# Performance work log

Measured on AMD Instinct MI355X. Metric: run time of the kernel, lower is better.

## Reference

```python
import jax, jax.numpy as jnp
import numpy as np

B, H, W, C = 8, 256, 256, 64
M1, M2 = 32, 32
SCALE = 1.0 / (C * C)


def setup_inputs() -> dict:
    key = jax.random.key(0)
    ku, k1, k2, k3, k4 = jax.random.split(key, 5)
    u = jax.random.normal(ku, (B, H, W, C), dtype=jnp.float32)
    wshape = (C, C, M1, M2)
    w_pos_r = SCALE * jax.random.normal(k1, wshape, dtype=jnp.float32)
    w_pos_i = SCALE * jax.random.normal(k2, wshape, dtype=jnp.float32)
    w_neg_r = SCALE * jax.random.normal(k3, wshape, dtype=jnp.float32)
    w_neg_i = SCALE * jax.random.normal(k4, wshape, dtype=jnp.float32)
    return {"u": u, "w_pos_r": w_pos_r, "w_pos_i": w_pos_i,
            "w_neg_r": w_neg_r, "w_neg_i": w_neg_i}


def _compl_mul2d(inp, weights):
    # inp: [B, m1, m2, Cin] complex; weights: [Cin, Cout, m1, m2] complex
    return jnp.einsum('bxyi,ioxy->bxyo', inp, weights)


def reference(u, w_pos_r, w_pos_i, w_neg_r, w_neg_i):
    b, h, w, c = u.shape
    wf = w // 2 + 1  # rfft size along W
    u_ft = jnp.fft.rfft2(u, axes=(1, 2))  # [B, H, Wf, C] complex
    w_pos = jax.lax.complex(w_pos_r, w_pos_i)
    w_neg = jax.lax.complex(w_neg_r, w_neg_i)
    top = _compl_mul2d(u_ft[:, :M1, :M2, :], w_pos)   # low positive freqs
    bot = _compl_mul2d(u_ft[:, h - M1:, :M2, :], w_neg)  # low negative freqs
    # out_ft zero-initialized, only truncated modes populated.
    # (Original allocates [B,H,W,C] but irfft2 with s=(H,W) only reads
    #  the first W//2+1 columns, which equals this [B,H,Wf,C] tensor.)
    out_ft = jnp.zeros((b, h, wf, c), dtype=u_ft.dtype)
    out_ft = out_ft.at[:, :M1, :M2, :].set(top)
    out_ft = out_ft.at[:, h - M1:, :M2, :].set(bot)
    # out_ft[:, -M1:M1] assignment in original is an empty slice (M1 <= H/2): no-op.
    return jnp.fft.irfft2(out_ft, s=(h, w), axes=(1, 2)).astype(u.dtype)
```

## Files before the change

### kernel.cpp

```cpp
#include <hip/hip_runtime.h>
#include <math.h>

#define BB 8
#define HH 256
#define WW 256
#define CC 64

__device__ inline void cmac(float2& a, float tx, float ty, float2 v) {
    a.x += tx * v.x - ty * v.y;
    a.y += tx * v.y + ty * v.x;
}
__device__ inline void fma4(float4& a, float s, float4 v) {
    a.x += s * v.x; a.y += s * v.y; a.z += s * v.z; a.w += s * v.w;
}

__global__ __launch_bounds__(256) void k_tw(float2* __restrict__ Tf,
                                            float2* __restrict__ Ti,
                                            float* __restrict__ Ty,
                                            float* __restrict__ T2) {
    int e = blockIdx.x * 256 + threadIdx.x;
    if (e < 16384) {
        int x = e >> 6;
        int j = e & 63;
        int kxa = j + ((j >> 5) * 192);
        int tt = (kxa * x) & 255;
        float ang = (float)tt * (6.283185307179586f / 256.0f);
        float s, c;
        sincosf(ang, &s, &c);
        Tf[(size_t)x * 64 + j] = make_float2(c, -s);
        const float k = 2.0f / 65536.0f;
        Ti[(size_t)j * 256 + x] = make_float2(c * k, s * k);
    } else {
        int f = e - 16384;
        if (f < 8192) {
            int yp = f >> 6;
            int col = f & 63;
            int par = (col >> 5) & 1;
            int cs = (col >> 4) & 1;
            int m = col & 15;
            int ky = 2 * m + par;
            int tt = (ky * yp) & 255;
            float ang = (float)tt * (6.283185307179586f / 256.0f);
            float s, c;
            sincosf(ang, &s, &c);
            Ty[f] = cs ? -s : c;
        } else {
            int g = f - 8192;
            int pi = g >> 12;
            int j = (g >> 7) & 31;
            int p = g & 127;
            int m = j >> 1, ri = j & 1;
            int ky = 2 * m + pi;
            int tt = (ky * p) & 255;
            float ang = (float)tt * (6.283185307179586f / 256.0f);
            float s, c;
            sincosf(ang, &s, &c);
            T2[g] = ri ? -s : c;
        }
    }
}

__global__ __launch_bounds__(256) void k_fwd_y(const float* __restrict__ u,
                                               const float* __restrict__ Ty,
                                               float2* __restrict__ V) {
    __shared__ float ue[4][16 * 68];
    __shared__ float uo[4][16 * 68];
    __shared__ float Tt[16 * 68];

    int t = threadIdx.x;
    int bx = blockIdx.x;
    int b = bx >> 6;
    int x4 = (bx & 63) * 4;
    int r = t >> 6;
    int l = t & 63;
    int x = x4 + r;
    int i8 = (l & 7) * 8;
    int w = l >> 3;
    int p = w & 1;
    int kq = w >> 1;
    int yy = l >> 2;
    int c0 = (l & 3) * 16;
    int trow = t >> 4;
    int tc = (t & 15) * 4;

    const float* ub = u + ((size_t)(b * HH + x)) * (WW * CC);
    const float* uplane = p ? uo[r] : ue[r];

    float4 aR[4], aI[4], bR[4], bI[4];
    #pragma unroll
    for (int m = 0; m < 4; ++m) {
        aR[m] = make_float4(0,0,0,0); aI[m] = make_float4(0,0,0,0);
        bR[m] = make_float4(0,0,0,0); bI[m] = make_float4(0,0,0,0);
    }

    for (int yt = 0; yt < 8; ++yt) {
        const float* plo = ub + (size_t)(yt * 16 + yy) * CC + c0;
        const float* phi = plo + 128 * CC;
        float4 l0 = *(const float4*)(plo);
        float4 l1 = *(const float4*)(plo + 4);
        float4 l2 = *(const float4*)(plo + 8);
        float4 l3 = *(const float4*)(plo + 12);
        float4 h0 = *(const float4*)(phi);
        float4 h1 = *(const float4*)(phi + 4);
        float4 h2 = *(const float4*)(phi + 8);
        float4 h3 = *(const float4*)(phi + 12);
        float4 tv = *(const float4*)(Ty + (size_t)(yt * 16 + trow) * 64 + tc);

        __syncthreads();
        int wb = yy * 68 + c0;
        float* uer = ue[r];
        float* uor = uo[r];
        *(float4*)(uer + wb)      = make_float4(l0.x+h0.x, l0.y+h0.y, l0.z+h0.z, l0.w+h0.w);
        *(float4*)(uer + wb + 4)  = make_float4(l1.x+h1.x, l1.y+h1.y, l1.z+h1.z, l1.w+h1.w);
        *(float4*)(uer + wb + 8)  = make_float4(l2.x+h2.x, l2.y+h2.y, l2.z+h2.z, l2.w+h2.w);
        *(float4*)(uer + wb + 12) = make_float4(l3.x+h3.x, l3.y+h3.y, l3.z+h3.z, l3.w+h3.w);
        *(float4*)(uor + wb)      = make_float4(l0.x-h0.x, l0.y-h0.y, l0.z-h0.z, l0.w-h0.w);
        *(float4*)(uor + wb + 4)  = make_float4(l1.x-h1.x, l1.y-h1.y, l1.z-h1.z, l1.w-h1.w);
        *(float4*)(uor + wb + 8)  = make_float4(l2.x-h2.x, l2.y-h2.y, l2.z-h2.z, l2.w-h2.w);
        *(float4*)(uor + wb + 12) = make_float4(l3.x-h3.x, l3.y-h3.y, l3.z-h3.z, l3.w-h3.w);
        *(float4*)(Tt + trow * 68 + tc) = tv;
        __syncthreads();

        #pragma unroll
        for (int y2 = 0; y2 < 16; ++y2) {
            const float* tb = Tt + y2 * 68 + p * 32 + kq * 2;
            float2 c01 = *(const float2*)(tb);
            float2 c89 = *(const float2*)(tb + 8);
            float2 s01 = *(const float2*)(tb + 16);
            float2 s89 = *(const float2*)(tb + 24);
            const float* up = uplane + y2 * 68 + i8;
            float4 u0 = *(const float4*)(up);
            float4 u1 = *(const float4*)(up + 4);
            fma4(aR[0], c01.x, u0);  fma4(bR[0], c01.x, u1);
            fma4(aI[0], s01.x, u0);  fma4(bI[0], s01.x, u1);
            fma4(aR[1], c01.y, u0);  fma4(bR[1], c01.y, u1);
            fma4(aI[1], s01.y, u0);  fma4(bI[1], s01.y, u1);
            fma4(aR[2], c89.x, u0);  fma4(bR[2], c89.x, u1);
            fma4(aI[2], s89.x, u0);  fma4(bI[2], s89.x, u1);
            fma4(aR[3], c89.y, u0);  fma4(bR[3], c89.y, u1);
            fma4(aI[3], s89.y, u0);  fma4(bI[3], s89.y, u1);
        }
    }

    int mv[4] = {2 * kq, 2 * kq + 1, 2 * kq + 8, 2 * kq + 9};
    #pragma unroll
    for (int mi = 0; mi < 4; ++mi) {
        int ky = 2 * mv[mi] + p;
        float2* vp = V + (size_t)(b * HH + x) * 2048 + ky * 64 + i8;
        *(float4*)(vp)     = make_float4(aR[mi].x, aI[mi].x, aR[mi].y, aI[mi].y);
        *(float4*)(vp + 2) = make_float4(aR[mi].z, aI[mi].z, aR[mi].w, aI[mi].w);
        *(float4*)(vp + 4) = make_float4(bR[mi].x, bI[mi].x, bR[mi].y, bI[mi].y);
        *(float4*)(vp + 6) = make_float4(bR[mi].z, bI[mi].z, bR[mi].w, bI[mi].w);
    }
}

__global__ __launch_bounds__(256) void k_fwd_x(const float2* __restrict__ Tf,
                                               const float2* __restrict__ V,
                                               float2* __restrict__ U) {
    __shared__ float sRe[2 * 2048];
    __shared__ float sIm[2 * 2048];
    __shared__ float2 Ts[32 * 16];

    int bx = blockIdx.x;
    int jq = bx >> 8;
    int ky = bx & 31;
    int b  = (bx >> 5) & 7;
    int t = threadIdx.x;
    int jr = t >> 5;
    int ir = t & 31;

    float2 a00 = {0,0}, a01 = {0,0}, a10 = {0,0}, a11 = {0,0};

    const float2* vb = V + (size_t)b * (HH * 2048) + ky * 64;
    int vrow = t >> 3;
    int vcol = (t & 7) * 8;
    int tjj = (t & 7) * 2;
    int parOff = (jr & 1) * 2048;

    for (int x0 = 0; x0 < 128; x0 += 32) {
        const float2* plo = vb + (size_t)(x0 + vrow) * 2048 + vcol;
        const float2* phi = plo + 128 * 2048;
        float4 l0 = *(const float4*)(plo);
        float4 l1 = *(const float4*)(plo + 2);
        float4 l2 = *(const float4*)(plo + 4);
        float4 l3 = *(const float4*)(plo + 6);
        float4 h0 = *(const float4*)(phi);
        float4 h1 = *(const float4*)(phi + 2);
        float4 h2 = *(const float4*)(phi + 4);
        float4 h3 = *(const float4*)(phi + 6);
        float4 tv = *(const float4*)(Tf + (size_t)(x0 + vrow) * 64 + jq * 16 + tjj);

        __syncthreads();
        *(float4*)&Ts[vrow * 16 + tjj] = tv;
        int wb = vrow * 64 + vcol;
        *(float4*)(sRe + wb)            = make_float4(l0.x+h0.x, l0.z+h0.z, l1.x+h1.x, l1.z+h1.z);
        *(float4*)(sRe + wb + 4)        = make_float4(l2.x+h2.x, l2.z+h2.z, l3.x+h3.x, l3.z+h3.z);
        *(float4*)(sIm + wb)            = make_float4(l0.y+h0.y, l0.w+h0.w, l1.y+h1.y, l1.w+h1.w);
        *(float4*)(sIm + wb + 4)        = make_float4(l2.y+h2.y, l2.w+h2.w, l3.y+h3.y, l3.w+h3.w);
        *(float4*)(sRe + 2048 + wb)     = make_float4(l0.x-h0.x, l0.z-h0.z, l1.x-h1.x, l1.z-h1.z);
        *(float4*)(sRe + 2048 + wb + 4) = make_float4(l2.x-h2.x, l2.z-h2.z, l3.x-h3.x, l3.z-h3.z);
        *(float4*)(sIm + 2048 + wb)     = make_float4(l0.y-h0.y, l0.w-h0.w, l1.y-h1.y, l1.w-h1.w);
        *(float4*)(sIm + 2048 + wb + 4) = make_float4(l2.y-h2.y, l2.w-h2.w, l3.y-h3.y, l3.w-h3.w);
        __syncthreads();

        #pragma unroll
        for (int xx = 0; xx < 32; ++xx) {
            float2 t0 = Ts[xx * 16 + jr];
            float2 t1 = Ts[xx * 16 + jr + 8];
            const float* re = sRe + parOff + xx * 64;
            const float* im = sIm + parOff + xx * 64;
            float vr0 = re[ir], vr1 = re[ir + 32];
            float vi0 = im[ir], vi1 = im[ir + 32];
            a00.x += t0.x*vr0 - t0.y*vi0;  a00.y += t0.x*vi0 + t0.y*vr0;
            a01.x += t0.x*vr1 - t0.y*vi1;  a01.y += t0.x*vi1 + t0.y*vr1;
            a10.x += t1.x*vr0 - t1.y*vi0;  a10.y += t1.x*vi0 + t1.y*vr0;
            a11.x += t1.x*vr1 - t1.y*vi1;  a11.y += t1.x*vi1 + t1.y*vr1;
        }
    }

    int j0 = jq * 16 + jr;
    float2* u0 = U + ((size_t)(j0 * 32 + ky) * 8 + b) * 64 + ir;
    u0[0]  = a00;
    u0[32] = a01;
    float2* u1 = U + ((size_t)((j0 + 8) * 32 + ky) * 8 + b) * 64 + ir;
    u1[0]  = a10;
    u1[32] = a11;
}

__global__ __launch_bounds__(256) void k_modew(const float* __restrict__ wpr,
                                               const float* __restrict__ wpi,
                                               const float* __restrict__ wnr,
                                               const float* __restrict__ wni,
                                               const float2* __restrict__ U,
                                               float2* __restrict__ OF) {
    __shared__ float2 uS[4 * 8 * 64];
    __shared__ float2 wS[4 * 8 * 32];

    int bx = blockIdx.x;
    int j   = bx & 63;
    int kyt = (bx >> 6) & 7;
    int oh  = bx >> 9;
    int ky0 = kyt * 4;
    int sel = j >> 5, kxl = j & 31;
    const float* sr = sel ? wnr : wpr;
    const float* si = sel ? wni : wpi;
    int tid = threadIdx.x;

    {
        const float4* up4 = (const float4*)(U + (size_t)(j * 32 + ky0) * 512);
        float4* uS4 = (float4*)uS;
        #pragma unroll
        for (int k = 0; k < 4; ++k) uS4[tid + 256 * k] = up4[tid + 256 * k];
    }

    int o32 = tid & 31;
    int bh  = tid >> 5;
    int irS = tid >> 5;
    int ooS = tid & 31;

    float2 acc[4];
    #pragma unroll
    for (int k = 0; k < 4; ++k) acc[k] = make_float2(0.f, 0.f);

    for (int it = 0; it < 8; ++it) {
        __syncthreads();
        {
            int ig = it * 8 + irS;
            int og = oh * 32 + ooS;
            size_t base = (((size_t)(ig * 64 + og)) * 32 + kxl) * 32 + ky0;
            float4 r0 = *(const float4*)(sr + base);
            float4 q0 = *(const float4*)(si + base);
            float2* wrow = wS + irS * 32 + ooS;
            wrow[0 * 256] = make_float2(r0.x, q0.x);
            wrow[1 * 256] = make_float2(r0.y, q0.y);
            wrow[2 * 256] = make_float2(r0.z, q0.z);
            wrow[3 * 256] = make_float2(r0.w, q0.w);
        }
        __syncthreads();
        #pragma unroll
        for (int ir = 0; ir < 8; ++ir) {
            int ig = it * 8 + ir;
            #pragma unroll
            for (int ky = 0; ky < 4; ++ky) {
                float2 wv = wS[ky * 256 + ir * 32 + o32];
                float2 uv = uS[ky * 512 + bh * 64 + ig];
                acc[ky].x += uv.x * wv.x - uv.y * wv.y;
                acc[ky].y += uv.x * wv.y + uv.y * wv.x;
            }
        }
    }

    int og = oh * 32 + o32;
    #pragma unroll
    for (int ky = 0; ky < 4; ++ky) {
        OF[((size_t)(bh * 32 + ky0 + ky) * 64 + j) * 64 + og] = acc[ky];
    }
}

__global__ __launch_bounds__(256) void k_inv_x(const float2* __restrict__ Ti,
                                               const float2* __restrict__ OF,
                                               float2* __restrict__ A) {
    __shared__ float2 Ts[32 * 32];
    __shared__ float2 Os[32 * 64];

    int bx = blockIdx.x;
    int xt = bx >> 8;
    int ky = bx & 31;
    int b  = (bx >> 5) & 7;
    int t = threadIdx.x;
    int or_ = t & 15;
    int xr = t >> 4;

    float2 acc[2][2][4];
    #pragma unroll
    for (int pa = 0; pa < 2; ++pa)
        #pragma unroll
        for (int p = 0; p < 2; ++p)
            #pragma unroll
            for (int q = 0; q < 4; ++q) acc[pa][p][q] = make_float2(0.f, 0.f);

    const float2* ofb = OF + (size_t)(b * 32 + ky) * 4096;
    int sj = t >> 3;
    int sx = (t & 7) * 4;
    int so = (t & 7) * 8;

    for (int kh = 0; kh < 2; ++kh) {
        const float2* tsrc = Ti + (size_t)(kh * 32 + sj) * 256 + xt * 32 + sx;
        float4 t0 = *(const float4*)(tsrc);
        float4 t1 = *(const float4*)(tsrc + 2);
        const float2* osrc = ofb + (size_t)(kh * 32 + sj) * 64 + so;
        float4 o0 = *(const float4*)(osrc);
        float4 o1 = *(const float4*)(osrc + 2);
        float4 o2 = *(const float4*)(osrc + 4);
        float4 o3 = *(const float4*)(osrc + 6);

        __syncthreads();
        *(float4*)&Ts[sj * 32 + sx]     = t0;
        *(float4*)&Ts[sj * 32 + sx + 2] = t1;
        float2* od = &Os[sj * 64 + so];
        *(float4*)(od)     = o0;
        *(float4*)(od + 2) = o1;
        *(float4*)(od + 4) = o2;
        *(float4*)(od + 6) = o3;
        __syncthreads();

        #pragma unroll
        for (int jj = 0; jj < 32; ++jj) {
            float4 tp = *(const float4*)&Ts[jj * 32 + xr * 2];
            float2 q0 = Os[jj * 64 + or_];
            float2 q1 = Os[jj * 64 + or_ + 16];
            float2 q2 = Os[jj * 64 + or_ + 32];
            float2 q3 = Os[jj * 64 + or_ + 48];
            const int pa = jj & 1;
            cmac(acc[pa][0][0], tp.x, tp.y, q0);
            cmac(acc[pa][0][1], tp.x, tp.y, q1);
            cmac(acc[pa][0][2], tp.x, tp.y, q2);
            cmac(acc[pa][0][3], tp.x, tp.y, q3);
            cmac(acc[pa][1][0], tp.z, tp.w, q0);
            cmac(acc[pa][1][1], tp.z, tp.w, q1);
            cmac(acc[pa][1][2], tp.z, tp.w, q2);
            cmac(acc[pa][1][3], tp.z, tp.w, q3);
        }
    }

    float sc = (ky == 0) ? 0.5f : 1.0f;
    #pragma unroll
    for (int p = 0; p < 2; ++p) {
        int x = xt * 32 + xr * 2 + p;
        float2* alo = A + ((size_t)(b * 256 + x) * 32 + ky) * 64 + or_;
        float2* ahi = A + ((size_t)(b * 256 + x + 128) * 32 + ky) * 64 + or_;
        #pragma unroll
        for (int q = 0; q < 4; ++q) {
            float2 se = acc[0][p][q], so2 = acc[1][p][q];
            alo[16 * q] = make_float2((se.x + so2.x) * sc, (se.y + so2.y) * sc);
            ahi[16 * q] = make_float2((se.x - so2.x) * sc, (se.y - so2.y) * sc);
        }
    }
}

__global__ __launch_bounds__(256) void k_inv_y(const float* __restrict__ T2g,
                                               const float2* __restrict__ A,
                                               float* __restrict__ out) {
    __shared__ float As[64 * 68];
    __shared__ float T2s[64 * 132];

    int t = threadIdx.x;
    int b = blockIdx.x >> 8;
    int x = blockIdx.x & 255;

    {
        int ky = t >> 3;
        int oc = (t & 7) * 8;
        const float2* ap = A + (size_t)(b * 256 + x) * 2048 + ky * 64 + oc;
        float4 g0 = *(const float4*)(ap);
        float4 g1 = *(const float4*)(ap + 2);
        float4 g2 = *(const float4*)(ap + 4);
        float4 g3 = *(const float4*)(ap + 6);
        int pi = ky & 1, m = ky >> 1;
        float* re = As + ((pi * 32) + 2 * m) * 68 + oc;
        float* im = As + ((pi * 32) + 2 * m + 1) * 68 + oc;
        *(float4*)(re)     = make_float4(g0.x, g0.z, g1.x, g1.z);
        *(float4*)(re + 4) = make_float4(g2.x, g2.z, g3.x, g3.z);
        *(float4*)(im)     = make_float4(g0.y, g0.w, g1.y, g1.w);
        *(float4*)(im + 4) = make_float4(g2.y, g2.w, g3.y, g3.w);
    }
    {
        int row = t >> 2;
        int c = (t & 3) * 32;
        const float* tg = T2g + (size_t)row * 128 + c;
        float* td = T2s + row * 132 + c;
        #pragma unroll
        for (int k = 0; k < 8; ++k) {
            float4 q = *(const float4*)(tg + 4 * k);
            *(float4*)(td + 4 * k) = q;
        }
    }
    __syncthreads();

    int pr = t >> 4;
    int o4 = (t & 15) * 4;

    float4 acc[2][8];
    #pragma unroll
    for (int pi = 0; pi < 2; ++pi)
        #pragma unroll
        for (int pp = 0; pp < 8; ++pp) acc[pi][pp] = make_float4(0,0,0,0);

    #pragma unroll
    for (int pi = 0; pi < 2; ++pi) {
        #pragma unroll
        for (int jj = 0; jj < 32; ++jj) {
            const float* trow = T2s + (pi * 32 + jj) * 132 + pr * 8;
            float4 ta = *(const float4*)(trow);
            float4 tb = *(const float4*)(trow + 4);
            float4 av = *(const float4*)(As + (pi * 32 + jj) * 68 + o4);
            fma4(acc[pi][0], ta.x, av);
            fma4(acc[pi][1], ta.y, av);
            fma4(acc[pi][2], ta.z, av);
            fma4(acc[pi][3], ta.w, av);
            fma4(acc[pi][4], tb.x, av);
            fma4(acc[pi][5], tb.y, av);
            fma4(acc[pi][6], tb.z, av);
            fma4(acc[pi][7], tb.w, av);
        }
    }

    float* op = out + (size_t)(b * 256 + x) * (256 * 64);
    #pragma unroll
    for (int pp = 0; pp < 8; ++pp) {
        int p = pr * 8 + pp;
        float4 e = acc[0][pp], d = acc[1][pp];
        *(float4*)(op + (size_t)p * 64 + o4)
            = make_float4(e.x+d.x, e.y+d.y, e.z+d.z, e.w+d.w);
        *(float4*)(op + (size_t)(p + 128) * 64 + o4)
            = make_float4(e.x-d.x, e.y-d.y, e.z-d.z, e.w-d.w);
    }
}

extern "C" void kernel_launch(void* const* d_in, const int* in_sizes, int n_in,
                              void* d_out, int out_size, void* d_ws, size_t ws_size,
                              hipStream_t stream) {
    const float* u   = (const float*)d_in[0];
    const float* wpr = (const float*)d_in[1];
    const float* wpi = (const float*)d_in[2];
    const float* wnr = (const float*)d_in[3];
    const float* wni = (const float*)d_in[4];
    float* out = (float*)d_out;

    char* ws = (char*)d_ws;
    float2* U  = (float2*)(ws);
    float2* OF = (float2*)(ws + 8388608);
    float2* V  = (float2*)(ws + 16777216);
    float2* A  = V;
    float2* Tf = (float2*)(ws + 50331648);
    float2* Ti = (float2*)(ws + 50331648 + 131072);
    float*  Ty = (float*)(ws + 50331648 + 262144);
    float*  T2 = (float*)(ws + 50331648 + 262144 + 32768);

    k_tw<<<128, 256, 0, stream>>>(Tf, Ti, Ty, T2);
    k_fwd_y<<<512, 256, 0, stream>>>(u, Ty, V);
    k_fwd_x<<<1024, 256, 0, stream>>>(Tf, V, U);
    k_modew<<<1024, 256, 0, stream>>>(wpr, wpi, wnr, wni, U, OF);
    k_inv_x<<<1024, 256, 0, stream>>>(Ti, OF, A);
    k_inv_y<<<BB * HH, 256, 0, stream>>>(T2, A, out);
}
```

Measured before the change: 220.8 us.

## Double-buffer shared tiles in forward y-DFT kernel with register prefetch

Restructures k_fwd_y so the next 8-row tile of input and twiddles is loaded into registers while the current tile is consumed from a second shared-memory buffer. This cuts the loop to one barrier per iteration and overlaps global loads with the FMA work. Tiles shrink from 16 to 8 rows, so there are twice as many iterations. Launch bounds now request 2 blocks per SM, which may constrain registers.

```diff
diff --git a/kernel.cpp b/kernel.cpp
--- a/kernel.cpp
+++ b/kernel.cpp
@@ -60,12 +60,12 @@
     }
 }
 
-__global__ __launch_bounds__(256) void k_fwd_y(const float* __restrict__ u,
-                                               const float* __restrict__ Ty,
-                                               float2* __restrict__ V) {
-    __shared__ float ue[4][16 * 68];
-    __shared__ float uo[4][16 * 68];
-    __shared__ float Tt[16 * 68];
+__global__ __launch_bounds__(256, 2) void k_fwd_y(const float* __restrict__ u,
+                                                  const float* __restrict__ Ty,
+                                                  float2* __restrict__ V) {
+    __shared__ float ue[2][4][8 * 68];
+    __shared__ float uo[2][4][8 * 68];
+    __shared__ float Tt[2][8 * 68];
 
     int t = threadIdx.x;
     int bx = blockIdx.x;
@@ -78,13 +78,12 @@
     int w = l >> 3;
     int p = w & 1;
     int kq = w >> 1;
-    int yy = l >> 2;
-    int c0 = (l & 3) * 16;
-    int trow = t >> 4;
-    int tc = (t & 15) * 4;
+    int yy = l >> 3;
+    int c0 = (l & 7) * 8;
+    int trow = t >> 5;
+    int tc = (t & 31) * 2;
 
     const float* ub = u + ((size_t)(b * HH + x)) * (WW * CC);
-    const float* uplane = p ? uo[r] : ue[r];
 
     float4 aR[4], aI[4], bR[4], bI[4];
     #pragma unroll
@@ -93,37 +92,45 @@
         bR[m] = make_float4(0,0,0,0); bI[m] = make_float4(0,0,0,0);
     }
 
-    for (int yt = 0; yt < 8; ++yt) {
-        const float* plo = ub + (size_t)(yt * 16 + yy) * CC + c0;
+    float4 L0, L1, H0, H1;
+    float2 TV;
+
+    {
+        const float* plo = ub + (size_t)yy * CC + c0;
         const float* phi = plo + 128 * CC;
-        float4 l0 = *(const float4*)(plo);
-        float4 l1 = *(const float4*)(plo + 4);
-        float4 l2 = *(const float4*)(plo + 8);
-        float4 l3 = *(const float4*)(plo + 12);
-        float4 h0 = *(const float4*)(phi);
-        float4 h1 = *(const float4*)(phi + 4);
-        float4 h2 = *(const float4*)(phi + 8);
-        float4 h3 = *(const float4*)(phi + 12);
-        float4 tv = *(const float4*)(Ty + (size_t)(yt * 16 + trow) * 64 + tc);
-
-        __syncthreads();
+        L0 = *(const float4*)(plo);
+        L1 = *(const float4*)(plo + 4);
+        H0 = *(const float4*)(phi);
+        H1 = *(const float4*)(phi + 4);
+        TV = *(const float2*)(Ty + (size_t)trow * 64 + tc);
         int wb = yy * 68 + c0;
-        float* uer = ue[r];
-        float* uor = uo[r];
-        *(float4*)(uer + wb)      = make_float4(l0.x+h0.x, l0.y+h0.y, l0.z+h0.z, l0.w+h0.w);
-        *(float4*)(uer + wb + 4)  = make_float4(l1.x+h1.x, l1.y+h1.y, l1.z+h1.z, l1.w+h1.w);
-        *(float4*)(uer + wb + 8)  = make_float4(l2.x+h2.x, l2.y+h2.y, l2.z+h2.z, l2.w+h2.w);
-        *(float4*)(uer + wb + 12) = make_float4(l3.x+h3.x, l3.y+h3.y, l3.z+h3.z, l3.w+h3.w);
-        *(float4*)(uor + wb)      = make_float4(l0.x-h0.x, l0.y-h0.y, l0.z-h0.z, l0.w-h0.w);
-        *(float4*)(uor + wb + 4)  = make_float4(l1.x-h1.x, l1.y-h1.y, l1.z-h1.z, l1.w-h1.w);
-        *(float4*)(uor + wb + 8)  = make_float4(l2.x-h2.x, l2.y-h2.y, l2.z-h2.z, l2.w-h2.w);
-        *(float4*)(uor + wb + 12) = make_float4(l3.x-h3.x, l3.y-h3.y, l3.z-h3.z, l3.w-h3.w);
-        *(float4*)(Tt + trow * 68 + tc) = tv;
-        __syncthreads();
-
-        #pragma unroll
-        for (int y2 = 0; y2 < 16; ++y2) {
-            const float* tb = Tt + y2 * 68 + p * 32 + kq * 2;
+        float* uer = ue[0][r];
+        float* uor = uo[0][r];
+        *(float4*)(uer + wb)     = make_float4(L0.x+H0.x, L0.y+H0.y, L0.z+H0.z, L0.w+H0.w);
+        *(float4*)(uer + wb + 4) = make_float4(L1.x+H1.x, L1.y+H1.y, L1.z+H1.z, L1.w+H1.w);
+        *(float4*)(uor + wb)     = make_float4(L0.x-H0.x, L0.y-H0.y, L0.z-H0.z, L0.w-H0.w);
+        *(float4*)(uor + wb + 4) = make_float4(L1.x-H1.x, L1.y-H1.y, L1.z-H1.z, L1.w-H1.w);
+        *(float2*)(&Tt[0][trow * 68 + tc]) = TV;
+    }
+    __syncthreads();
+
+    for (int yt = 0; yt < 16; ++yt) {
+        int cur = yt & 1;
+        if (yt < 15) {
+            const float* plo = ub + (size_t)((yt + 1) * 8 + yy) * CC + c0;
+            const float* phi = plo + 128 * CC;
+            L0 = *(const float4*)(plo);
+            L1 = *(const float4*)(plo + 4);
+            H0 = *(const float4*)(phi);
+            H1 = *(const float4*)(phi + 4);
+            TV = *(const float2*)(Ty + (size_t)((yt + 1) * 8 + trow) * 64 + tc);
+        }
+
+        const float* uplane = p ? uo[cur][r] : ue[cur][r];
+        const float* ttab = Tt[cur];
+        #pragma unroll
+        for (int y2 = 0; y2 < 8; ++y2) {
+            const float* tb = ttab + y2 * 68 + p * 32 + kq * 2;
             float2 c01 = *(const float2*)(tb);
             float2 c89 = *(const float2*)(tb + 8);
             float2 s01 = *(const float2*)(tb + 16);
@@ -140,6 +147,19 @@
             fma4(aR[3], c89.y, u0);  fma4(bR[3], c89.y, u1);
             fma4(aI[3], s89.y, u0);  fma4(bI[3], s89.y, u1);
         }
+
+        if (yt < 15) {
+            int nb = cur ^ 1;
+            int wb = yy * 68 + c0;
+            float* uer = ue[nb][r];
+            float* uor = uo[nb][r];
+            *(float4*)(uer + wb)     = make_float4(L0.x+H0.x, L0.y+H0.y, L0.z+H0.z, L0.w+H0.w);
+            *(float4*)(uer + wb + 4) = make_float4(L1.x+H1.x, L1.y+H1.y, L1.z+H1.z, L1.w+H1.w);
+            *(float4*)(uor + wb)     = make_float4(L0.x-H0.x, L0.y-H0.y, L0.z-H0.z, L0.w-H0.w);
+            *(float4*)(uor + wb + 4) = make_float4(L1.x-H1.x, L1.y-H1.y, L1.z-H1.z, L1.w-H1.w);
+            *(float2*)(&Tt[nb][trow * 68 + tc]) = TV;
+        }
+        __syncthreads();
     }
 
     int mv[4] = {2 * kq, 2 * kq + 1, 2 * kq + 8, 2 * kq + 9};
```

Measured after the change: 217.5 us. No clear change (-1.5%).
